# Optimization experiments

Hardware: AMD Instinct MI355X
Metric: run time of the kernel (lower is better)

Reference implementation:

```python
import jax, jax.numpy as jnp
import numpy as np

MAX_REL = 16  # max_relative_position (keys == values)


def _relative_positions(T, max_pos):
    r = jnp.arange(T)
    dist = r[None, :] - r[:, None]          # [T, T], k - q
    return jnp.clip(dist, -max_pos, max_pos) + max_pos


def setup_inputs() -> dict:
    key = jax.random.key(0)
    ks = jax.random.split(key, 5)
    B, H, T, D = 4, 16, 1024, 64
    V = 2 * MAX_REL + 1
    return {
        "q": jax.random.normal(ks[0], (B, H, T, D), jnp.float32),
        "k": jax.random.normal(ks[1], (B, H, T, D), jnp.float32),
        "v": jax.random.normal(ks[2], (B, H, T, D), jnp.float32),
        "emb_k": jax.random.normal(ks[3], (V, D), jnp.float32),
        "emb_v": jax.random.normal(ks[4], (V, D), jnp.float32),
    }


def reference(q, k, v, emb_k, emb_v):
    # q,k,v: [B,H,T,D]; emb_*: [2*MAX_REL+1, D]
    T = q.shape[2]
    D = k.shape[-1]
    rel_idx = _relative_positions(T, MAX_REL)          # [T,T]
    rel_k = emb_k[rel_idx]                             # [T,T,D]
    rel_v = emb_v[rel_idx]                             # [T,T,D]

    # content-content + content-position logits
    logits = jnp.einsum('bhtd,bhsd->bhts', q, k)
    logits = logits + jnp.einsum('bhtd,tsd->bhts', q, rel_k)
    logits = logits * (1.0 / jnp.sqrt(jnp.float32(D)))

    attn = jax.nn.softmax(logits, axis=-1)             # [B,H,T,T]
    out = jnp.einsum('bhts,bhsd->bhtd', attn, v)
    out = out + jnp.einsum('bhts,tsd->bhtd', attn, rel_v)
    return out, attn
```

## Files before the change

### kernel.cpp

```cpp
#include <hip/hip_runtime.h>
#include <hip/hip_bf16.h>

#define TT 1024
#define DD 64
#define MAXREL 16
#define NV 33
#define QBLK 16
#define SCALE 0.125f
#define BH 64

typedef short bf16x8 __attribute__((ext_vector_type(8)));
typedef short bf16x4 __attribute__((ext_vector_type(4)));
typedef float f32x4 __attribute__((ext_vector_type(4)));

#define SBAR() __builtin_amdgcn_sched_barrier(0)
#define WAITV(N)   __builtin_amdgcn_s_waitcnt(0x0F70 | (N))
#define WAITLGKM() __builtin_amdgcn_s_waitcnt(0xC07F)

static __device__ inline void gload16(const void* g, void* l) {
    __builtin_amdgcn_global_load_lds(
        (const __attribute__((address_space(1))) void*)g,
        (__attribute__((address_space(3))) void*)l, 16, 0, 0);
}

static __device__ inline short f2bf(float f) {
    __hip_bfloat16 h = __float2bfloat16(f);
    return *(short*)&h;
}
static __device__ inline float bf2f(short s) {
    union { unsigned u; float f; } x;
    x.u = ((unsigned)(unsigned short)s) << 16;
    return x.f;
}
static __device__ inline bf16x8 pack8(float4 a, float4 b) {
    bf16x8 r;
    r[0]=f2bf(a.x); r[1]=f2bf(a.y); r[2]=f2bf(a.z); r[3]=f2bf(a.w);
    r[4]=f2bf(b.x); r[5]=f2bf(b.y); r[6]=f2bf(b.z); r[7]=f2bf(b.w);
    return r;
}

__global__ __launch_bounds__(256)
void convk_kernel(const float* __restrict__ src, short* __restrict__ dst) {
    size_t i = (size_t)blockIdx.x * 256 + threadIdx.x;
    const float4* s = (const float4*)(src + i * 8);
    *(bf16x8*)(dst + i * 8) = pack8(s[0], s[1]);
}

__global__ __launch_bounds__(256)
void transv_kernel(const float* __restrict__ v, short* __restrict__ vt) {
    int bh = blockIdx.x >> 4;
    int st = blockIdx.x & 15;
    int wave = threadIdx.x >> 6, lane = threadIdx.x & 63;
    int s0 = st * 64 + wave * 16;
    const float* vp = v + ((size_t)bh * TT + s0) * DD + lane;
    bf16x8 lo, hi;
    #pragma unroll
    for (int e = 0; e < 8; ++e) lo[e] = f2bf(vp[(size_t)e * DD]);
    #pragma unroll
    for (int e = 0; e < 8; ++e) hi[e] = f2bf(vp[(size_t)(e + 8) * DD]);
    short* dp = vt + ((size_t)bh * DD + lane) * TT + s0;
    *(bf16x8*)dp = lo;
    *(bf16x8*)(dp + 8) = hi;
}

__global__ __launch_bounds__(512)
void relattn_kernel(const float* __restrict__ q_g,
                    const short* __restrict__ kb,
                    const short* __restrict__ vt,
                    const float* __restrict__ ek_g,
                    const float* __restrict__ ev_g,
                    float* __restrict__ out_g,
                    float* __restrict__ attn_g) {
    __shared__ __align__(16) char pbuf[QBLK * 2048];
    __shared__ __align__(16) char kstage[8 * 4096];
    __shared__ float pair_lds[4][16][16];
    __shared__ float qe_lds[QBLK * NV];
    __shared__ float w_lds[QBLK * NV];
    __shared__ float psum_lds[QBLK][8];
    __shared__ float psuf_lds[QBLK][8];
    __shared__ float pmid_lds[QBLK][8];
    __shared__ float inv_lds[QBLK];

    const int t    = threadIdx.x;
    const int bid  = blockIdx.x;
    const int wg   = ((bid & 7) << 9) | (bid >> 3);
    const int bh   = wg >> 6;
    const int q0   = (wg & 63) * QBLK;
    const int w    = t >> 6;
    const int lane = t & 63;
    const int lr   = lane & 15;
    const int akg  = lane >> 4;
    const int srl  = lane >> 3;
    const int sqg  = (lane & 7) ^ srl;

    const short* kgbase = kb + (size_t)bh * TT * DD;
    char* kst = kstage + w * 4096;

    auto KSTAGE = [&](int B, int NT) {
        const int s0 = w * 128 + NT * 16;
        gload16(kgbase + (size_t)(s0 + srl) * 64 + sqg * 8,     kst + B * 2048);
        gload16(kgbase + (size_t)(s0 + 8 + srl) * 64 + sqg * 8, kst + B * 2048 + 1024);
    };

    bf16x8 qF0, qF1;
    {
        const float* qp = q_g + ((size_t)bh * TT + q0 + lr) * DD + akg * 8;
        float4 a = *(const float4*)qp,        b = *(const float4*)(qp + 4);
        float4 c = *(const float4*)(qp + 32), d = *(const float4*)(qp + 36);
        qF0 = pack8(a, b); qF1 = pack8(c, d);
    }

    KSTAGE(0, 0); KSTAGE(1, 1);

    for (int i = t; i < QBLK * NV; i += 512) w_lds[i] = 0.f;
    if (w < 3) {
        int v = w * 16 + lr; if (v > 32) v = 32;
        const float* ep = ek_g + v * DD + akg * 8;
        float4 a = *(const float4*)ep,        b = *(const float4*)(ep + 4);
        float4 c = *(const float4*)(ep + 32), d = *(const float4*)(ep + 36);
        bf16x8 eF0 = pack8(a, b), eF1 = pack8(c, d);
        f32x4 qacc = {0.f, 0.f, 0.f, 0.f};
        qacc = __builtin_amdgcn_mfma_f32_16x16x32_bf16(eF0, qF0, qacc, 0, 0, 0);
        qacc = __builtin_amdgcn_mfma_f32_16x16x32_bf16(eF1, qF1, qacc, 0, 0, 0);
        #pragma unroll
        for (int j = 0; j < 4; ++j) {
            int vv = w * 16 + akg * 4 + j;
            if (vv < NV) qe_lds[lr * NV + vv] = __expf(qacc[j] * SCALE);
        }
    }
    __syncthreads();

    {
        const int tq = q0 + lr;
        const int X  = (lr & 7) << 4;
        const float eqe_lo = qe_lds[lr * NV];
        const float eqe_hi = qe_lds[lr * NV + 32];
        float sum = 0.f, suff = 0.f, msum = 0.f;

        auto CVALU = [&](f32x4 acc, int nt) {
            const int sb = w * 128 + nt * 16 + akg * 4;
            float ex0 = __expf(acc[0] * SCALE), ex1 = __expf(acc[1] * SCALE);
            float ex2 = __expf(acc[2] * SCALE), ex3 = __expf(acc[3] * SCALE);
            float e0, e1, e2, e3;
            if (sb >= tq + MAXREL) {
                e0 = ex0 * eqe_hi; e1 = ex1 * eqe_hi;
                e2 = ex2 * eqe_hi; e3 = ex3 * eqe_hi;
                float csum = (e0 + e1) + (e2 + e3);
                sum += csum; suff += csum;
            } else if (sb + 3 <= tq - MAXREL) {
                e0 = ex0 * eqe_lo; e1 = ex1 * eqe_lo;
                e2 = ex2 * eqe_lo; e3 = ex3 * eqe_lo;
                sum += (e0 + e1) + (e2 + e3);
            } else {
                float ee[4]; float exs[4] = {ex0, ex1, ex2, ex3};
                #pragma unroll
                for (int j = 0; j < 4; ++j) {
                    int dr = sb + j - tq;
                    int dc = dr < -MAXREL ? -MAXREL : (dr > MAXREL ? MAXREL : dr);
                    float v = exs[j] * qe_lds[lr * NV + dc + MAXREL];
                    ee[j] = v;
                    sum += v;
                    if (dr >= MAXREL) suff += v;
                    if (dr > -MAXREL && dr < MAXREL) {
                        w_lds[lr * NV + dr + MAXREL] = v;
                        msum += v;
                    }
                }
                e0 = ee[0]; e1 = ee[1]; e2 = ee[2]; e3 = ee[3];
            }
            bf16x4 p4;
            p4[0] = f2bf(e0); p4[1] = f2bf(e1);
            p4[2] = f2bf(e2); p4[3] = f2bf(e3);
            *(bf16x4*)(pbuf + lr * 2048 + ((2 * sb) ^ X)) = p4;
        };

        auto MFMA2 = [&](bf16x8 kf0, bf16x8 kf1) {
            f32x4 acc = {0.f, 0.f, 0.f, 0.f};
            acc = __builtin_amdgcn_mfma_f32_16x16x32_bf16(kf0, qF0, acc, 0, 0, 0);
            acc = __builtin_amdgcn_mfma_f32_16x16x32_bf16(kf1, qF1, acc, 0, 0, 0);
            return acc;
        };

        f32x4 aA, aB;
        #define CITER(B, NT, W, PF, AC, AP, NP) \
            WAITV(W); SBAR(); \
            { bf16x8 kf0 = *(const bf16x8*)(kst + (B)*2048 + lr*128 + ((((akg))  ^(lr&7)) << 4)); \
              bf16x8 kf1 = *(const bf16x8*)(kst + (B)*2048 + lr*128 + ((((akg)+4)^(lr&7)) << 4)); \
              if ((NP) >= 0) CVALU(AP, NP); \
              WAITLGKM(); SBAR(); \
              if (PF) KSTAGE((B), (NT) + 2); \
              AC = MFMA2(kf0, kf1); } \
            SBAR()
        CITER(0, 0, 2, 1, aA, aB, -1);
        CITER(1, 1, 2, 1, aB, aA,  0);
        CITER(0, 2, 2, 1, aA, aB,  1);
        CITER(1, 3, 2, 1, aB, aA,  2);
        CITER(0, 4, 2, 1, aA, aB,  3);
        CITER(1, 5, 2, 1, aB, aA,  4);
        CITER(0, 6, 2, 0, aA, aB,  5);
        CITER(1, 7, 0, 0, aB, aA,  6);
        CVALU(aB, 7);
        #undef CITER

        {
            WAITLGKM(); SBAR();
            const short* vgbase = vt + ((size_t)bh * DD + (w & 3) * 16) * TT;
            const int S0 = (w >> 2) * 8;
            gload16(vgbase + (size_t)srl * TT + S0 * 64 + sqg * 8,           kst);
            gload16(vgbase + (size_t)(8 + srl) * TT + S0 * 64 + sqg * 8,     kst + 1024);
            gload16(vgbase + (size_t)srl * TT + (S0 + 1) * 64 + sqg * 8,     kst + 2048);
            gload16(vgbase + (size_t)(8 + srl) * TT + (S0 + 1) * 64 + sqg * 8, kst + 3072);
        }

        sum  += __shfl_xor(sum, 16);  sum  += __shfl_xor(sum, 32);
        suff += __shfl_xor(suff, 16); suff += __shfl_xor(suff, 32);
        msum += __shfl_xor(msum, 16); msum += __shfl_xor(msum, 32);
        if (lane < 16) {
            psum_lds[lr][w] = sum;
            psuf_lds[lr][w] = suff;
            pmid_lds[lr][w] = msum;
        }
    }
    __syncthreads();

    if (t < QBLK) {
        float s = 0.f, sf = 0.f, sm = 0.f;
        #pragma unroll
        for (int i = 0; i < 8; ++i) {
            s  += psum_lds[t][i];
            sf += psuf_lds[t][i];
            sm += pmid_lds[t][i];
        }
        inv_lds[t] = 1.0f / s;
        w_lds[t * NV]      = s - sf - sm;
        w_lds[t * NV + 32] = sf;
    }
    __syncthreads();

    {
        const int dt = w & 3;
        const int sh = w >> 2;
        const int S0 = sh * 8;
        const int lc = lane & 15;
        const int dcol = dt * 16 + lc;
        const char* pb = pbuf + lc * 2048;
        const int X = (lc & 7) << 4;
        char* vst = kst;
        const short* vgbase = vt + ((size_t)bh * DD + dt * 16) * TT;
        f32x4 acc0 = {0.f, 0.f, 0.f, 0.f};
        f32x4 acc1 = {0.f, 0.f, 0.f, 0.f};

        auto VSTAGE = [&](int B, int S) {
            gload16(vgbase + (size_t)srl * TT + S * 64 + sqg * 8,       vst + B * 2048);
            gload16(vgbase + (size_t)(8 + srl) * TT + S * 64 + sqg * 8, vst + B * 2048 + 1024);
        };

        #define FITER(B, S, W, PF, AC) \
            WAITV(W); SBAR(); \
            { bf16x8 vf0 = *(const bf16x8*)(vst + (B)*2048 + lc*128 + ((((akg))  ^(lc&7)) << 4)); \
              bf16x8 vf1 = *(const bf16x8*)(vst + (B)*2048 + lc*128 + ((((akg)+4)^(lc&7)) << 4)); \
              bf16x8 a0 = *(const bf16x8*)(pb + (((2*(S))*64     + akg*16) ^ X)); \
              bf16x8 a1 = *(const bf16x8*)(pb + (((2*(S)+1)*64   + akg*16) ^ X)); \
              WAITLGKM(); SBAR(); \
              if (PF) VSTAGE((B), (S) + 2); \
              AC = __builtin_amdgcn_mfma_f32_16x16x32_bf16(a0, vf0, AC, 0, 0, 0); \
              AC = __builtin_amdgcn_mfma_f32_16x16x32_bf16(a1, vf1, AC, 0, 0, 0); } \
            SBAR()
        FITER(0, S0 + 0, 2, 1, acc0);  FITER(1, S0 + 1, 2, 1, acc1);
        FITER(0, S0 + 2, 2, 1, acc0);  FITER(1, S0 + 3, 2, 1, acc1);
        FITER(0, S0 + 4, 2, 1, acc0);  FITER(1, S0 + 5, 2, 1, acc1);
        FITER(0, S0 + 6, 2, 0, acc0);  FITER(1, S0 + 7, 0, 0, acc1);
        #undef FITER

        f32x4 acc;
        acc[0] = acc0[0] + acc1[0]; acc[1] = acc0[1] + acc1[1];
        acc[2] = acc0[2] + acc1[2]; acc[3] = acc0[3] + acc1[3];

        if (sh == 1) {
            #pragma unroll
            for (int j = 0; j < 4; ++j)
                pair_lds[dt][akg * 4 + j][lc] = acc[j];
        }
        __syncthreads();

        if (sh == 0) {
            const int rb = akg * 4;
            float o0 = acc[0] + pair_lds[dt][rb + 0][lc];
            float o1 = acc[1] + pair_lds[dt][rb + 1][lc];
            float o2 = acc[2] + pair_lds[dt][rb + 2][lc];
            float o3 = acc[3] + pair_lds[dt][rb + 3][lc];
            #pragma unroll 8
            for (int v = 0; v < NV; ++v) {
                float ev = ev_g[v * DD + dcol];
                o0 += w_lds[(rb + 0) * NV + v] * ev;
                o1 += w_lds[(rb + 1) * NV + v] * ev;
                o2 += w_lds[(rb + 2) * NV + v] * ev;
                o3 += w_lds[(rb + 3) * NV + v] * ev;
            }
            float* op = out_g + ((size_t)bh * TT + q0 + rb) * DD + dcol;
            op[0 * DD] = o0 * inv_lds[rb + 0];
            op[1 * DD] = o1 * inv_lds[rb + 1];
            op[2 * DD] = o2 * inv_lds[rb + 2];
            op[3 * DD] = o3 * inv_lds[rb + 3];
        }
    }

    {
        float* ab = attn_g + ((size_t)bh * TT + q0) * TT;
        #pragma unroll
        for (int j = 0; j < 2; ++j) {
            const int r = w * 2 + j;
            const float inv = inv_lds[r];
            const int X = (r & 7) << 4;
            #pragma unroll
            for (int i = 0; i < 4; ++i) {
                bf16x4 p4 = *(const bf16x4*)(pbuf + r * 2048 + ((8 * lane + 512 * i) ^ X));
                f32x4 o;
                o[0] = bf2f(p4[0]) * inv; o[1] = bf2f(p4[1]) * inv;
                o[2] = bf2f(p4[2]) * inv; o[3] = bf2f(p4[3]) * inv;
                __builtin_nontemporal_store(o, (f32x4*)(ab + (size_t)r * TT + lane * 4 + 256 * i));
            }
        }
    }
}

extern "C" void kernel_launch(void* const* d_in, const int* in_sizes, int n_in,
                              void* d_out, int out_size, void* d_ws, size_t ws_size,
                              hipStream_t stream) {
    const float* q  = (const float*)d_in[0];
    const float* k  = (const float*)d_in[1];
    const float* v  = (const float*)d_in[2];
    const float* ek = (const float*)d_in[3];
    const float* ev = (const float*)d_in[4];
    float* out  = (float*)d_out;
    float* attn = out + (size_t)BH * TT * DD;

    short* kbuf = (short*)d_ws;
    short* vtb  = kbuf + (size_t)BH * TT * DD;

    convk_kernel<<<dim3(2048), dim3(256), 0, stream>>>(k, kbuf);
    transv_kernel<<<dim3(1024), dim3(256), 0, stream>>>(v, vtb);
    relattn_kernel<<<dim3(4096), dim3(512), 0, stream>>>(q, kbuf, vtb, ek, ev, out, attn);
}
```

Before: 118.9 us.

## Replace LDS-staged K/V pipelines with direct global fragment loads for higher occupancy

```diff
diff --git a/kernel.cpp b/kernel.cpp
--- a/kernel.cpp
+++ b/kernel.cpp
@@ -12,16 +12,6 @@
 typedef short bf16x8 __attribute__((ext_vector_type(8)));
 typedef short bf16x4 __attribute__((ext_vector_type(4)));
 typedef float f32x4 __attribute__((ext_vector_type(4)));
-
-#define SBAR() __builtin_amdgcn_sched_barrier(0)
-#define WAITV(N)   __builtin_amdgcn_s_waitcnt(0x0F70 | (N))
-#define WAITLGKM() __builtin_amdgcn_s_waitcnt(0xC07F)
-
-static __device__ inline void gload16(const void* g, void* l) {
-    __builtin_amdgcn_global_load_lds(
-        (const __attribute__((address_space(1))) void*)g,
-        (__attribute__((address_space(3))) void*)l, 16, 0, 0);
-}
 
 static __device__ inline short f2bf(float f) {
     __hip_bfloat16 h = __float2bfloat16(f);
@@ -63,7 +53,7 @@
     *(bf16x8*)(dp + 8) = hi;
 }
 
-__global__ __launch_bounds__(512)
+__global__ __launch_bounds__(512, 8)
 void relattn_kernel(const float* __restrict__ q_g,
                     const short* __restrict__ kb,
                     const short* __restrict__ vt,
@@ -72,8 +62,7 @@
                     float* __restrict__ out_g,
                     float* __restrict__ attn_g) {
     __shared__ __align__(16) char pbuf[QBLK * 2048];
-    __shared__ __align__(16) char kstage[8 * 4096];
-    __shared__ float pair_lds[4][16][16];
+    __shared__ short pair_lds[4][16][16];
     __shared__ float qe_lds[QBLK * NV];
     __shared__ float w_lds[QBLK * NV];
     __shared__ float psum_lds[QBLK][8];
@@ -90,17 +79,6 @@
     const int lane = t & 63;
     const int lr   = lane & 15;
     const int akg  = lane >> 4;
-    const int srl  = lane >> 3;
-    const int sqg  = (lane & 7) ^ srl;
-
-    const short* kgbase = kb + (size_t)bh * TT * DD;
-    char* kst = kstage + w * 4096;
-
-    auto KSTAGE = [&](int B, int NT) {
-        const int s0 = w * 128 + NT * 16;
-        gload16(kgbase + (size_t)(s0 + srl) * 64 + sqg * 8,     kst + B * 2048);
-        gload16(kgbase + (size_t)(s0 + 8 + srl) * 64 + sqg * 8, kst + B * 2048 + 1024);
-    };
 
     bf16x8 qF0, qF1;
     {
@@ -109,8 +87,6 @@
         float4 c = *(const float4*)(qp + 32), d = *(const float4*)(qp + 36);
         qF0 = pack8(a, b); qF1 = pack8(c, d);
     }
-
-    KSTAGE(0, 0); KSTAGE(1, 1);
 
     for (int i = t; i < QBLK * NV; i += 512) w_lds[i] = 0.f;
     if (w < 3) {
@@ -131,13 +107,18 @@
     __syncthreads();
 
     {
+        const short* kp0 = kb + (size_t)bh * TT * DD
+                         + (size_t)(w * 128 + lr) * DD + akg * 8;
         const int tq = q0 + lr;
         const int X  = (lr & 7) << 4;
         const float eqe_lo = qe_lds[lr * NV];
         const float eqe_hi = qe_lds[lr * NV + 32];
         float sum = 0.f, suff = 0.f, msum = 0.f;
 
-        auto CVALU = [&](f32x4 acc, int nt) {
+        auto CCOMP = [&](bf16x8 kf0, bf16x8 kf1, int nt) {
+            f32x4 acc = {0.f, 0.f, 0.f, 0.f};
+            acc = __builtin_amdgcn_mfma_f32_16x16x32_bf16(kf0, qF0, acc, 0, 0, 0);
+            acc = __builtin_amdgcn_mfma_f32_16x16x32_bf16(kf1, qF1, acc, 0, 0, 0);
             const int sb = w * 128 + nt * 16 + akg * 4;
             float ex0 = __expf(acc[0] * SCALE), ex1 = __expf(acc[1] * SCALE);
             float ex2 = __expf(acc[2] * SCALE), ex3 = __expf(acc[3] * SCALE);
@@ -174,43 +155,20 @@
             *(bf16x4*)(pbuf + lr * 2048 + ((2 * sb) ^ X)) = p4;
         };
 
-        auto MFMA2 = [&](bf16x8 kf0, bf16x8 kf1) {
-            f32x4 acc = {0.f, 0.f, 0.f, 0.f};
-            acc = __builtin_amdgcn_mfma_f32_16x16x32_bf16(kf0, qF0, acc, 0, 0, 0);
-            acc = __builtin_amdgcn_mfma_f32_16x16x32_bf16(kf1, qF1, acc, 0, 0, 0);
-            return acc;
-        };
-
-        f32x4 aA, aB;
-        #define CITER(B, NT, W, PF, AC, AP, NP) \
-            WAITV(W); SBAR(); \
-            { bf16x8 kf0 = *(const bf16x8*)(kst + (B)*2048 + lr*128 + ((((akg))  ^(lr&7)) << 4)); \
-              bf16x8 kf1 = *(const bf16x8*)(kst + (B)*2048 + lr*128 + ((((akg)+4)^(lr&7)) << 4)); \
-              if ((NP) >= 0) CVALU(AP, NP); \
-              WAITLGKM(); SBAR(); \
-              if (PF) KSTAGE((B), (NT) + 2); \
-              AC = MFMA2(kf0, kf1); } \
-            SBAR()
-        CITER(0, 0, 2, 1, aA, aB, -1);
-        CITER(1, 1, 2, 1, aB, aA,  0);
-        CITER(0, 2, 2, 1, aA, aB,  1);
-        CITER(1, 3, 2, 1, aB, aA,  2);
-        CITER(0, 4, 2, 1, aA, aB,  3);
-        CITER(1, 5, 2, 1, aB, aA,  4);
-        CITER(0, 6, 2, 0, aA, aB,  5);
-        CITER(1, 7, 0, 0, aB, aA,  6);
-        CVALU(aB, 7);
-        #undef CITER
-
-        {
-            WAITLGKM(); SBAR();
-            const short* vgbase = vt + ((size_t)bh * DD + (w & 3) * 16) * TT;
-            const int S0 = (w >> 2) * 8;
-            gload16(vgbase + (size_t)srl * TT + S0 * 64 + sqg * 8,           kst);
-            gload16(vgbase + (size_t)(8 + srl) * TT + S0 * 64 + sqg * 8,     kst + 1024);
-            gload16(vgbase + (size_t)srl * TT + (S0 + 1) * 64 + sqg * 8,     kst + 2048);
-            gload16(vgbase + (size_t)(8 + srl) * TT + (S0 + 1) * 64 + sqg * 8, kst + 3072);
-        }
+        bf16x8 kA0, kA1, kB0, kB1;
+        #define KLD(R0, R1, NT) \
+            R0 = *(const bf16x8*)(kp0 + (NT) * 1024); \
+            R1 = *(const bf16x8*)(kp0 + (NT) * 1024 + 32)
+        KLD(kA0, kA1, 0); KLD(kB0, kB1, 1);
+        CCOMP(kA0, kA1, 0); KLD(kA0, kA1, 2);
+        CCOMP(kB0, kB1, 1); KLD(kB0, kB1, 3);
+        CCOMP(kA0, kA1, 2); KLD(kA0, kA1, 4);
+        CCOMP(kB0, kB1, 3); KLD(kB0, kB1, 5);
+        CCOMP(kA0, kA1, 4); KLD(kA0, kA1, 6);
+        CCOMP(kB0, kB1, 5); KLD(kB0, kB1, 7);
+        CCOMP(kA0, kA1, 6);
+        CCOMP(kB0, kB1, 7);
+        #undef KLD
 
         sum  += __shfl_xor(sum, 16);  sum  += __shfl_xor(sum, 32);
         suff += __shfl_xor(suff, 16); suff += __shfl_xor(suff, 32);
@@ -240,37 +198,29 @@
     {
         const int dt = w & 3;
         const int sh = w >> 2;
-        const int S0 = sh * 8;
         const int lc = lane & 15;
         const int dcol = dt * 16 + lc;
         const char* pb = pbuf + lc * 2048;
         const int X = (lc & 7) << 4;
-        char* vst = kst;
-        const short* vgbase = vt + ((size_t)bh * DD + dt * 16) * TT;
+        const short* vb = vt + ((size_t)bh * DD + dcol) * TT + sh * 512 + akg * 8;
         f32x4 acc0 = {0.f, 0.f, 0.f, 0.f};
         f32x4 acc1 = {0.f, 0.f, 0.f, 0.f};
 
-        auto VSTAGE = [&](int B, int S) {
-            gload16(vgbase + (size_t)srl * TT + S * 64 + sqg * 8,       vst + B * 2048);
-            gload16(vgbase + (size_t)(8 + srl) * TT + S * 64 + sqg * 8, vst + B * 2048 + 1024);
-        };
-
-        #define FITER(B, S, W, PF, AC) \
-            WAITV(W); SBAR(); \
-            { bf16x8 vf0 = *(const bf16x8*)(vst + (B)*2048 + lc*128 + ((((akg))  ^(lc&7)) << 4)); \
-              bf16x8 vf1 = *(const bf16x8*)(vst + (B)*2048 + lc*128 + ((((akg)+4)^(lc&7)) << 4)); \
-              bf16x8 a0 = *(const bf16x8*)(pb + (((2*(S))*64     + akg*16) ^ X)); \
-              bf16x8 a1 = *(const bf16x8*)(pb + (((2*(S)+1)*64   + akg*16) ^ X)); \
-              WAITLGKM(); SBAR(); \
-              if (PF) VSTAGE((B), (S) + 2); \
-              AC = __builtin_amdgcn_mfma_f32_16x16x32_bf16(a0, vf0, AC, 0, 0, 0); \
-              AC = __builtin_amdgcn_mfma_f32_16x16x32_bf16(a1, vf1, AC, 0, 0, 0); } \
-            SBAR()
-        FITER(0, S0 + 0, 2, 1, acc0);  FITER(1, S0 + 1, 2, 1, acc1);
-        FITER(0, S0 + 2, 2, 1, acc0);  FITER(1, S0 + 3, 2, 1, acc1);
-        FITER(0, S0 + 4, 2, 1, acc0);  FITER(1, S0 + 5, 2, 1, acc1);
-        FITER(0, S0 + 6, 2, 0, acc0);  FITER(1, S0 + 7, 0, 0, acc1);
-        #undef FITER
+        #pragma unroll
+        for (int g = 0; g < 4; ++g) {
+            bf16x8 v0 = *(const bf16x8*)(vb + (4*g+0) * 32);
+            bf16x8 v1 = *(const bf16x8*)(vb + (4*g+1) * 32);
+            bf16x8 v2 = *(const bf16x8*)(vb + (4*g+2) * 32);
+            bf16x8 v3 = *(const bf16x8*)(vb + (4*g+3) * 32);
+            bf16x8 a0 = *(const bf16x8*)(pb + ((sh*1024 + (4*g+0)*64 + akg*16) ^ X));
+            bf16x8 a1 = *(const bf16x8*)(pb + ((sh*1024 + (4*g+1)*64 + akg*16) ^ X));
+            bf16x8 a2 = *(const bf16x8*)(pb + ((sh*1024 + (4*g+2)*64 + akg*16) ^ X));
+            bf16x8 a3 = *(const bf16x8*)(pb + ((sh*1024 + (4*g+3)*64 + akg*16) ^ X));
+            acc0 = __builtin_amdgcn_mfma_f32_16x16x32_bf16(a0, v0, acc0, 0, 0, 0);
+            acc1 = __builtin_amdgcn_mfma_f32_16x16x32_bf16(a1, v1, acc1, 0, 0, 0);
+            acc0 = __builtin_amdgcn_mfma_f32_16x16x32_bf16(a2, v2, acc0, 0, 0, 0);
+            acc1 = __builtin_amdgcn_mfma_f32_16x16x32_bf16(a3, v3, acc1, 0, 0, 0);
+        }
 
         f32x4 acc;
         acc[0] = acc0[0] + acc1[0]; acc[1] = acc0[1] + acc1[1];
@@ -279,16 +229,16 @@
         if (sh == 1) {
             #pragma unroll
             for (int j = 0; j < 4; ++j)
-                pair_lds[dt][akg * 4 + j][lc] = acc[j];
+                pair_lds[dt][akg * 4 + j][lc] = f2bf(acc[j]);
         }
         __syncthreads();
 
         if (sh == 0) {
             const int rb = akg * 4;
-            float o0 = acc[0] + pair_lds[dt][rb + 0][lc];
-            float o1 = acc[1] + pair_lds[dt][rb + 1][lc];
-            float o2 = acc[2] + pair_lds[dt][rb + 2][lc];
-            float o3 = acc[3] + pair_lds[dt][rb + 3][lc];
+            float o0 = acc[0] + bf2f(pair_lds[dt][rb + 0][lc]);
+            float o1 = acc[1] + bf2f(pair_lds[dt][rb + 1][lc]);
+            float o2 = acc[2] + bf2f(pair_lds[dt][rb + 2][lc]);
+            float o3 = acc[3] + bf2f(pair_lds[dt][rb + 3][lc]);
             #pragma unroll 8
             for (int v = 0; v < NV; ++v) {
                 float ev = ev_g[v * DD + dcol];
```

Result: slower. 167.3 us (+40.7%).

## Shrink LDS footprint with single-buffered staging and bf16 scratch to raise occupancy

Applied to the files above, without the earlier changes.

```diff
diff --git a/kernel.cpp b/kernel.cpp
--- a/kernel.cpp
+++ b/kernel.cpp
@@ -14,7 +14,7 @@
 typedef float f32x4 __attribute__((ext_vector_type(4)));
 
 #define SBAR() __builtin_amdgcn_sched_barrier(0)
-#define WAITV(N)   __builtin_amdgcn_s_waitcnt(0x0F70 | (N))
+#define WAITV0()   __builtin_amdgcn_s_waitcnt(0x0F70)
 #define WAITLGKM() __builtin_amdgcn_s_waitcnt(0xC07F)
 
 static __device__ inline void gload16(const void* g, void* l) {
@@ -63,7 +63,7 @@
     *(bf16x8*)(dp + 8) = hi;
 }
 
-__global__ __launch_bounds__(512)
+__global__ __launch_bounds__(512, 6)
 void relattn_kernel(const float* __restrict__ q_g,
                     const short* __restrict__ kb,
                     const short* __restrict__ vt,
@@ -72,13 +72,13 @@
                     float* __restrict__ out_g,
                     float* __restrict__ attn_g) {
     __shared__ __align__(16) char pbuf[QBLK * 2048];
-    __shared__ __align__(16) char kstage[8 * 4096];
-    __shared__ float pair_lds[4][16][16];
-    __shared__ float qe_lds[QBLK * NV];
-    __shared__ float w_lds[QBLK * NV];
-    __shared__ float psum_lds[QBLK][8];
-    __shared__ float psuf_lds[QBLK][8];
-    __shared__ float pmid_lds[QBLK][8];
+    __shared__ __align__(16) char kstage[8 * 2048];
+    __shared__ short pair_lds[4][16][16];
+    __shared__ short qe_lds[QBLK * NV];
+    __shared__ short w_lds[QBLK * NV];
+    __shared__ short psum_lds[QBLK][8];
+    __shared__ short psuf_lds[QBLK][8];
+    __shared__ short pmid_lds[QBLK][8];
     __shared__ float inv_lds[QBLK];
 
     const int t    = threadIdx.x;
@@ -94,12 +94,12 @@
     const int sqg  = (lane & 7) ^ srl;
 
     const short* kgbase = kb + (size_t)bh * TT * DD;
-    char* kst = kstage + w * 4096;
-
-    auto KSTAGE = [&](int B, int NT) {
+    char* kst = kstage + w * 2048;
+
+    auto KSTAGE = [&](int NT) {
         const int s0 = w * 128 + NT * 16;
-        gload16(kgbase + (size_t)(s0 + srl) * 64 + sqg * 8,     kst + B * 2048);
-        gload16(kgbase + (size_t)(s0 + 8 + srl) * 64 + sqg * 8, kst + B * 2048 + 1024);
+        gload16(kgbase + (size_t)(s0 + srl) * 64 + sqg * 8,     kst);
+        gload16(kgbase + (size_t)(s0 + 8 + srl) * 64 + sqg * 8, kst + 1024);
     };
 
     bf16x8 qF0, qF1;
@@ -110,9 +110,9 @@
         qF0 = pack8(a, b); qF1 = pack8(c, d);
     }
 
-    KSTAGE(0, 0); KSTAGE(1, 1);
-
-    for (int i = t; i < QBLK * NV; i += 512) w_lds[i] = 0.f;
+    KSTAGE(0);
+
+    for (int i = t; i < QBLK * NV; i += 512) w_lds[i] = 0;
     if (w < 3) {
         int v = w * 16 + lr; if (v > 32) v = 32;
         const float* ep = ek_g + v * DD + akg * 8;
@@ -125,7 +125,7 @@
         #pragma unroll
         for (int j = 0; j < 4; ++j) {
             int vv = w * 16 + akg * 4 + j;
-            if (vv < NV) qe_lds[lr * NV + vv] = __expf(qacc[j] * SCALE);
+            if (vv < NV) qe_lds[lr * NV + vv] = f2bf(__expf(qacc[j] * SCALE));
         }
     }
     __syncthreads();
@@ -133,8 +133,8 @@
     {
         const int tq = q0 + lr;
         const int X  = (lr & 7) << 4;
-        const float eqe_lo = qe_lds[lr * NV];
-        const float eqe_hi = qe_lds[lr * NV + 32];
+        const float eqe_lo = bf2f(qe_lds[lr * NV]);
+        const float eqe_hi = bf2f(qe_lds[lr * NV + 32]);
         float sum = 0.f, suff = 0.f, msum = 0.f;
 
         auto CVALU = [&](f32x4 acc, int nt) {
@@ -157,12 +157,12 @@
                 for (int j = 0; j < 4; ++j) {
                     int dr = sb + j - tq;
                     int dc = dr < -MAXREL ? -MAXREL : (dr > MAXREL ? MAXREL : dr);
-                    float v = exs[j] * qe_lds[lr * NV + dc + MAXREL];
+                    float v = exs[j] * bf2f(qe_lds[lr * NV + dc + MAXREL]);
                     ee[j] = v;
                     sum += v;
                     if (dr >= MAXREL) suff += v;
                     if (dr > -MAXREL && dr < MAXREL) {
-                        w_lds[lr * NV + dr + MAXREL] = v;
+                        w_lds[lr * NV + dr + MAXREL] = f2bf(v);
                         msum += v;
                     }
                 }
@@ -182,43 +182,40 @@
         };
 
         f32x4 aA, aB;
-        #define CITER(B, NT, W, PF, AC, AP, NP) \
-            WAITV(W); SBAR(); \
-            { bf16x8 kf0 = *(const bf16x8*)(kst + (B)*2048 + lr*128 + ((((akg))  ^(lr&7)) << 4)); \
-              bf16x8 kf1 = *(const bf16x8*)(kst + (B)*2048 + lr*128 + ((((akg)+4)^(lr&7)) << 4)); \
+        #define CITER(NT, PF, AC, AP, NP) \
+            WAITV0(); SBAR(); \
+            { bf16x8 kf0 = *(const bf16x8*)(kst + lr*128 + ((((akg))  ^(lr&7)) << 4)); \
+              bf16x8 kf1 = *(const bf16x8*)(kst + lr*128 + ((((akg)+4)^(lr&7)) << 4)); \
               if ((NP) >= 0) CVALU(AP, NP); \
               WAITLGKM(); SBAR(); \
-              if (PF) KSTAGE((B), (NT) + 2); \
+              if (PF) KSTAGE((NT) + 1); \
               AC = MFMA2(kf0, kf1); } \
             SBAR()
-        CITER(0, 0, 2, 1, aA, aB, -1);
-        CITER(1, 1, 2, 1, aB, aA,  0);
-        CITER(0, 2, 2, 1, aA, aB,  1);
-        CITER(1, 3, 2, 1, aB, aA,  2);
-        CITER(0, 4, 2, 1, aA, aB,  3);
-        CITER(1, 5, 2, 1, aB, aA,  4);
-        CITER(0, 6, 2, 0, aA, aB,  5);
-        CITER(1, 7, 0, 0, aB, aA,  6);
+        CITER(0, 1, aA, aB, -1);
+        CITER(1, 1, aB, aA,  0);
+        CITER(2, 1, aA, aB,  1);
+        CITER(3, 1, aB, aA,  2);
+        CITER(4, 1, aA, aB,  3);
+        CITER(5, 1, aB, aA,  4);
+        CITER(6, 1, aA, aB,  5);
+        CITER(7, 0, aB, aA,  6);
         CVALU(aB, 7);
         #undef CITER
 
         {
-            WAITLGKM(); SBAR();
             const short* vgbase = vt + ((size_t)bh * DD + (w & 3) * 16) * TT;
             const int S0 = (w >> 2) * 8;
-            gload16(vgbase + (size_t)srl * TT + S0 * 64 + sqg * 8,           kst);
-            gload16(vgbase + (size_t)(8 + srl) * TT + S0 * 64 + sqg * 8,     kst + 1024);
-            gload16(vgbase + (size_t)srl * TT + (S0 + 1) * 64 + sqg * 8,     kst + 2048);
-            gload16(vgbase + (size_t)(8 + srl) * TT + (S0 + 1) * 64 + sqg * 8, kst + 3072);
+            gload16(vgbase + (size_t)srl * TT + S0 * 64 + sqg * 8,       kst);
+            gload16(vgbase + (size_t)(8 + srl) * TT + S0 * 64 + sqg * 8, kst + 1024);
         }
 
         sum  += __shfl_xor(sum, 16);  sum  += __shfl_xor(sum, 32);
         suff += __shfl_xor(suff, 16); suff += __shfl_xor(suff, 32);
         msum += __shfl_xor(msum, 16); msum += __shfl_xor(msum, 32);
         if (lane < 16) {
-            psum_lds[lr][w] = sum;
-            psuf_lds[lr][w] = suff;
-            pmid_lds[lr][w] = msum;
+            psum_lds[lr][w] = f2bf(sum);
+            psuf_lds[lr][w] = f2bf(suff);
+            pmid_lds[lr][w] = f2bf(msum);
         }
     }
     __syncthreads();
@@ -227,13 +224,13 @@
         float s = 0.f, sf = 0.f, sm = 0.f;
         #pragma unroll
         for (int i = 0; i < 8; ++i) {
-            s  += psum_lds[t][i];
-            sf += psuf_lds[t][i];
-            sm += pmid_lds[t][i];
+            s  += bf2f(psum_lds[t][i]);
+            sf += bf2f(psuf_lds[t][i]);
+            sm += bf2f(pmid_lds[t][i]);
         }
         inv_lds[t] = 1.0f / s;
-        w_lds[t * NV]      = s - sf - sm;
-        w_lds[t * NV + 32] = sf;
+        w_lds[t * NV]      = f2bf(s - sf - sm);
+        w_lds[t * NV + 32] = f2bf(sf);
     }
     __syncthreads();
 
@@ -250,26 +247,26 @@
         f32x4 acc0 = {0.f, 0.f, 0.f, 0.f};
         f32x4 acc1 = {0.f, 0.f, 0.f, 0.f};
 
-        auto VSTAGE = [&](int B, int S) {
-            gload16(vgbase + (size_t)srl * TT + S * 64 + sqg * 8,       vst + B * 2048);
-            gload16(vgbase + (size_t)(8 + srl) * TT + S * 64 + sqg * 8, vst + B * 2048 + 1024);
+        auto VSTAGE = [&](int S) {
+            gload16(vgbase + (size_t)srl * TT + S * 64 + sqg * 8,       vst);
+            gload16(vgbase + (size_t)(8 + srl) * TT + S * 64 + sqg * 8, vst + 1024);
         };
 
-        #define FITER(B, S, W, PF, AC) \
-            WAITV(W); SBAR(); \
-            { bf16x8 vf0 = *(const bf16x8*)(vst + (B)*2048 + lc*128 + ((((akg))  ^(lc&7)) << 4)); \
-              bf16x8 vf1 = *(const bf16x8*)(vst + (B)*2048 + lc*128 + ((((akg)+4)^(lc&7)) << 4)); \
+        #define FITER(S, PF, AC) \
+            WAITV0(); SBAR(); \
+            { bf16x8 vf0 = *(const bf16x8*)(vst + lc*128 + ((((akg))  ^(lc&7)) << 4)); \
+              bf16x8 vf1 = *(const bf16x8*)(vst + lc*128 + ((((akg)+4)^(lc&7)) << 4)); \
               bf16x8 a0 = *(const bf16x8*)(pb + (((2*(S))*64     + akg*16) ^ X)); \
               bf16x8 a1 = *(const bf16x8*)(pb + (((2*(S)+1)*64   + akg*16) ^ X)); \
               WAITLGKM(); SBAR(); \
-              if (PF) VSTAGE((B), (S) + 2); \
+              if (PF) VSTAGE((S) + 1); \
               AC = __builtin_amdgcn_mfma_f32_16x16x32_bf16(a0, vf0, AC, 0, 0, 0); \
               AC = __builtin_amdgcn_mfma_f32_16x16x32_bf16(a1, vf1, AC, 0, 0, 0); } \
             SBAR()
-        FITER(0, S0 + 0, 2, 1, acc0);  FITER(1, S0 + 1, 2, 1, acc1);
-        FITER(0, S0 + 2, 2, 1, acc0);  FITER(1, S0 + 3, 2, 1, acc1);
-        FITER(0, S0 + 4, 2, 1, acc0);  FITER(1, S0 + 5, 2, 1, acc1);
-        FITER(0, S0 + 6, 2, 0, acc0);  FITER(1, S0 + 7, 0, 0, acc1);
+        FITER(S0 + 0, 1, acc0);  FITER(S0 + 1, 1, acc1);
+        FITER(S0 + 2, 1, acc0);  FITER(S0 + 3, 1, acc1);
+        FITER(S0 + 4, 1, acc0);  FITER(S0 + 5, 1, acc1);
+        FITER(S0 + 6, 1, acc0);  FITER(S0 + 7, 0, acc1);
         #undef FITER
 
         f32x4 acc;
@@ -279,23 +276,23 @@
         if (sh == 1) {
             #pragma unroll
             for (int j = 0; j < 4; ++j)
-                pair_lds[dt][akg * 4 + j][lc] = acc[j];
+                pair_lds[dt][akg * 4 + j][lc] = f2bf(acc[j]);
         }
         __syncthreads();
 
         if (sh == 0) {
             const int rb = akg * 4;
-            float o0 = acc[0] + pair_lds[dt][rb + 0][lc];
-            float o1 = acc[1] + pair_lds[dt][rb + 1][lc];
-            float o2 = acc[2] + pair_lds[dt][rb + 2][lc];
-            float o3 = acc[3] + pair_lds[dt][rb + 3][lc];
+            float o0 = acc[0] + bf2f(pair_lds[dt][rb + 0][lc]);
+            float o1 = acc[1] + bf2f(pair_lds[dt][rb + 1][lc]);
+            float o2 = acc[2] + bf2f(pair_lds[dt][rb + 2][lc]);
+            float o3 = acc[3] + bf2f(pair_lds[dt][rb + 3][lc]);
             #pragma unroll 8
             for (int v = 0; v < NV; ++v) {
                 float ev = ev_g[v * DD + dcol];
-                o0 += w_lds[(rb + 0) * NV + v] * ev;
-                o1 += w_lds[(rb + 1) * NV + v] * ev;
-                o2 += w_lds[(rb + 2) * NV + v] * ev;
-                o3 += w_lds[(rb + 3) * NV + v] * ev;
+                o0 += bf2f(w_lds[(rb + 0) * NV + v]) * ev;
+                o1 += bf2f(w_lds[(rb + 1) * NV + v]) * ev;
+                o2 += bf2f(w_lds[(rb + 2) * NV + v]) * ev;
+                o3 += bf2f(w_lds[(rb + 3) * NV + v]) * ev;
             }
             float* op = out_g + ((size_t)bh * TT + q0 + rb) * DD + dcol;
             op[0 * DD] = o0 * inv_lds[rb + 0];
```

After: 132.1 us. +11.1%, slower.

## Keep softmax probabilities in registers and feed PV MFMA via lane shuffles

Applied to the files above, without the earlier changes.

```diff
diff --git a/kernel.cpp b/kernel.cpp
--- a/kernel.cpp
+++ b/kernel.cpp
@@ -31,6 +31,9 @@
     union { unsigned u; float f; } x;
     x.u = ((unsigned)(unsigned short)s) << 16;
     return x.f;
+}
+static __device__ inline unsigned pk2(float lo, float hi) {
+    return (unsigned)(unsigned short)f2bf(lo) | ((unsigned)(unsigned short)f2bf(hi) << 16);
 }
 static __device__ inline bf16x8 pack8(float4 a, float4 b) {
     bf16x8 r;
@@ -63,7 +66,7 @@
     *(bf16x8*)(dp + 8) = hi;
 }
 
-__global__ __launch_bounds__(512)
+__global__ __launch_bounds__(512, 6)
 void relattn_kernel(const float* __restrict__ q_g,
                     const short* __restrict__ kb,
                     const short* __restrict__ vt,
@@ -71,9 +74,7 @@
                     const float* __restrict__ ev_g,
                     float* __restrict__ out_g,
                     float* __restrict__ attn_g) {
-    __shared__ __align__(16) char pbuf[QBLK * 2048];
     __shared__ __align__(16) char kstage[8 * 4096];
-    __shared__ float pair_lds[4][16][16];
     __shared__ float qe_lds[QBLK * NV];
     __shared__ float w_lds[QBLK * NV];
     __shared__ float psum_lds[QBLK][8];
@@ -130,14 +131,15 @@
     }
     __syncthreads();
 
+    uint2 pP0, pP1, pP2, pP3, pP4, pP5, pP6, pP7;
+
     {
         const int tq = q0 + lr;
-        const int X  = (lr & 7) << 4;
         const float eqe_lo = qe_lds[lr * NV];
         const float eqe_hi = qe_lds[lr * NV + 32];
         float sum = 0.f, suff = 0.f, msum = 0.f;
 
-        auto CVALU = [&](f32x4 acc, int nt) {
+        auto CVALU = [&](f32x4 acc, int nt) -> uint2 {
             const int sb = w * 128 + nt * 16 + akg * 4;
             float ex0 = __expf(acc[0] * SCALE), ex1 = __expf(acc[1] * SCALE);
             float ex2 = __expf(acc[2] * SCALE), ex3 = __expf(acc[3] * SCALE);
@@ -168,10 +170,10 @@
                 }
                 e0 = ee[0]; e1 = ee[1]; e2 = ee[2]; e3 = ee[3];
             }
-            bf16x4 p4;
-            p4[0] = f2bf(e0); p4[1] = f2bf(e1);
-            p4[2] = f2bf(e2); p4[3] = f2bf(e3);
-            *(bf16x4*)(pbuf + lr * 2048 + ((2 * sb) ^ X)) = p4;
+            uint2 r;
+            r.x = pk2(e0, e1);
+            r.y = pk2(e2, e3);
+            return r;
         };
 
         auto MFMA2 = [&](bf16x8 kf0, bf16x8 kf1) {
@@ -182,35 +184,25 @@
         };
 
         f32x4 aA, aB;
-        #define CITER(B, NT, W, PF, AC, AP, NP) \
+        #define CITER(B, NT, W, PF, AC, AP, NP, PD) \
             WAITV(W); SBAR(); \
             { bf16x8 kf0 = *(const bf16x8*)(kst + (B)*2048 + lr*128 + ((((akg))  ^(lr&7)) << 4)); \
               bf16x8 kf1 = *(const bf16x8*)(kst + (B)*2048 + lr*128 + ((((akg)+4)^(lr&7)) << 4)); \
-              if ((NP) >= 0) CVALU(AP, NP); \
+              if ((NP) >= 0) PD = CVALU(AP, NP); \
               WAITLGKM(); SBAR(); \
               if (PF) KSTAGE((B), (NT) + 2); \
               AC = MFMA2(kf0, kf1); } \
             SBAR()
-        CITER(0, 0, 2, 1, aA, aB, -1);
-        CITER(1, 1, 2, 1, aB, aA,  0);
-        CITER(0, 2, 2, 1, aA, aB,  1);
-        CITER(1, 3, 2, 1, aB, aA,  2);
-        CITER(0, 4, 2, 1, aA, aB,  3);
-        CITER(1, 5, 2, 1, aB, aA,  4);
-        CITER(0, 6, 2, 0, aA, aB,  5);
-        CITER(1, 7, 0, 0, aB, aA,  6);
-        CVALU(aB, 7);
+        CITER(0, 0, 2, 1, aA, aB, -1, pP0);
+        CITER(1, 1, 2, 1, aB, aA,  0, pP0);
+        CITER(0, 2, 2, 1, aA, aB,  1, pP1);
+        CITER(1, 3, 2, 1, aB, aA,  2, pP2);
+        CITER(0, 4, 2, 1, aA, aB,  3, pP3);
+        CITER(1, 5, 2, 1, aB, aA,  4, pP4);
+        CITER(0, 6, 2, 0, aA, aB,  5, pP5);
+        CITER(1, 7, 0, 0, aB, aA,  6, pP6);
+        pP7 = CVALU(aB, 7);
         #undef CITER
-
-        {
-            WAITLGKM(); SBAR();
-            const short* vgbase = vt + ((size_t)bh * DD + (w & 3) * 16) * TT;
-            const int S0 = (w >> 2) * 8;
-            gload16(vgbase + (size_t)srl * TT + S0 * 64 + sqg * 8,           kst);
-            gload16(vgbase + (size_t)(8 + srl) * TT + S0 * 64 + sqg * 8,     kst + 1024);
-            gload16(vgbase + (size_t)srl * TT + (S0 + 1) * 64 + sqg * 8,     kst + 2048);
-            gload16(vgbase + (size_t)(8 + srl) * TT + (S0 + 1) * 64 + sqg * 8, kst + 3072);
-        }
 
         sum  += __shfl_xor(sum, 16);  sum  += __shfl_xor(sum, 32);
         suff += __shfl_xor(suff, 16); suff += __shfl_xor(suff, 32);
@@ -238,88 +230,76 @@
     __syncthreads();
 
     {
-        const int dt = w & 3;
-        const int sh = w >> 2;
-        const int S0 = sh * 8;
-        const int lc = lane & 15;
-        const int dcol = dt * 16 + lc;
-        const char* pb = pbuf + lc * 2048;
-        const int X = (lc & 7) << 4;
-        char* vst = kst;
-        const short* vgbase = vt + ((size_t)bh * DD + dt * 16) * TT;
-        f32x4 acc0 = {0.f, 0.f, 0.f, 0.f};
-        f32x4 acc1 = {0.f, 0.f, 0.f, 0.f};
-
-        auto VSTAGE = [&](int B, int S) {
-            gload16(vgbase + (size_t)srl * TT + S * 64 + sqg * 8,       vst + B * 2048);
-            gload16(vgbase + (size_t)(8 + srl) * TT + S * 64 + sqg * 8, vst + B * 2048 + 1024);
+        const float invr = inv_lds[lr];
+        float* ab = attn_g + ((size_t)(bh * TT + q0 + lr)) * TT + w * 128;
+        f32x4 acc0 = {0.f,0.f,0.f,0.f}, acc1 = {0.f,0.f,0.f,0.f};
+        f32x4 acc2 = {0.f,0.f,0.f,0.f}, acc3 = {0.f,0.f,0.f,0.f};
+        const int srcA = lr + ((akg & 1) << 5);
+        const int srcB = srcA + 16;
+        const bool useO = akg >= 2;
+        const short* vbase = vt + ((size_t)bh * DD + lr) * TT + w * 128 + akg * 8;
+
+        auto PVCHUNK = [&](uint2 E, uint2 O, int S) {
+            unsigned ex0 = (unsigned)__shfl((int)E.x, srcA), ey0 = (unsigned)__shfl((int)E.y, srcA);
+            unsigned ex1 = (unsigned)__shfl((int)E.x, srcB), ey1 = (unsigned)__shfl((int)E.y, srcB);
+            unsigned ox0 = (unsigned)__shfl((int)O.x, srcA), oy0 = (unsigned)__shfl((int)O.y, srcA);
+            unsigned ox1 = (unsigned)__shfl((int)O.x, srcB), oy1 = (unsigned)__shfl((int)O.y, srcB);
+            union { unsigned u[4]; bf16x8 v; } af;
+            af.u[0] = useO ? ox0 : ex0;
+            af.u[1] = useO ? oy0 : ey0;
+            af.u[2] = useO ? ox1 : ex1;
+            af.u[3] = useO ? oy1 : ey1;
+            const short* vb = vbase + S * 32;
+            bf16x8 v0 = *(const bf16x8*)(vb);
+            bf16x8 v1 = *(const bf16x8*)(vb + 16 * TT);
+            bf16x8 v2 = *(const bf16x8*)(vb + 32 * TT);
+            bf16x8 v3 = *(const bf16x8*)(vb + 48 * TT);
+            acc0 = __builtin_amdgcn_mfma_f32_16x16x32_bf16(af.v, v0, acc0, 0, 0, 0);
+            acc1 = __builtin_amdgcn_mfma_f32_16x16x32_bf16(af.v, v1, acc1, 0, 0, 0);
+            acc2 = __builtin_amdgcn_mfma_f32_16x16x32_bf16(af.v, v2, acc2, 0, 0, 0);
+            acc3 = __builtin_amdgcn_mfma_f32_16x16x32_bf16(af.v, v3, acc3, 0, 0, 0);
+            f32x4 o;
+            o[0] = bf2f((short)(E.x & 0xffff)) * invr;
+            o[1] = bf2f((short)(E.x >> 16))    * invr;
+            o[2] = bf2f((short)(E.y & 0xffff)) * invr;
+            o[3] = bf2f((short)(E.y >> 16))    * invr;
+            __builtin_nontemporal_store(o, (f32x4*)(ab + (2*S)*16 + akg*4));
+            o[0] = bf2f((short)(O.x & 0xffff)) * invr;
+            o[1] = bf2f((short)(O.x >> 16))    * invr;
+            o[2] = bf2f((short)(O.y & 0xffff)) * invr;
+            o[3] = bf2f((short)(O.y >> 16))    * invr;
+            __builtin_nontemporal_store(o, (f32x4*)(ab + (2*S+1)*16 + akg*4));
         };
 
-        #define FITER(B, S, W, PF, AC) \
-            WAITV(W); SBAR(); \
-            { bf16x8 vf0 = *(const bf16x8*)(vst + (B)*2048 + lc*128 + ((((akg))  ^(lc&7)) << 4)); \
-              bf16x8 vf1 = *(const bf16x8*)(vst + (B)*2048 + lc*128 + ((((akg)+4)^(lc&7)) << 4)); \
-              bf16x8 a0 = *(const bf16x8*)(pb + (((2*(S))*64     + akg*16) ^ X)); \
-              bf16x8 a1 = *(const bf16x8*)(pb + (((2*(S)+1)*64   + akg*16) ^ X)); \
-              WAITLGKM(); SBAR(); \
-              if (PF) VSTAGE((B), (S) + 2); \
-              AC = __builtin_amdgcn_mfma_f32_16x16x32_bf16(a0, vf0, AC, 0, 0, 0); \
-              AC = __builtin_amdgcn_mfma_f32_16x16x32_bf16(a1, vf1, AC, 0, 0, 0); } \
-            SBAR()
-        FITER(0, S0 + 0, 2, 1, acc0);  FITER(1, S0 + 1, 2, 1, acc1);
-        FITER(0, S0 + 2, 2, 1, acc0);  FITER(1, S0 + 3, 2, 1, acc1);
-        FITER(0, S0 + 4, 2, 1, acc0);  FITER(1, S0 + 5, 2, 1, acc1);
-        FITER(0, S0 + 6, 2, 0, acc0);  FITER(1, S0 + 7, 0, 0, acc1);
-        #undef FITER
-
-        f32x4 acc;
-        acc[0] = acc0[0] + acc1[0]; acc[1] = acc0[1] + acc1[1];
-        acc[2] = acc0[2] + acc1[2]; acc[3] = acc0[3] + acc1[3];
-
-        if (sh == 1) {
+        PVCHUNK(pP0, pP1, 0);
+        PVCHUNK(pP2, pP3, 1);
+        PVCHUNK(pP4, pP5, 2);
+        PVCHUNK(pP6, pP7, 3);
+
+        float* pw = (float*)kstage + w * 1024;
+        #pragma unroll
+        for (int j = 0; j < 4; ++j) {
+            pw[(akg*4 + j) * 64 +  0 + lr] = acc0[j];
+            pw[(akg*4 + j) * 64 + 16 + lr] = acc1[j];
+            pw[(akg*4 + j) * 64 + 32 + lr] = acc2[j];
+            pw[(akg*4 + j) * 64 + 48 + lr] = acc3[j];
+        }
+    }
+    __syncthreads();
+
+    {
+        const int d = t & 63;
+        const float* pr = (const float*)kstage;
+        #pragma unroll
+        for (int h = 0; h < 2; ++h) {
+            const int r = (t >> 6) + h * 8;
+            float o = 0.f;
             #pragma unroll
-            for (int j = 0; j < 4; ++j)
-                pair_lds[dt][akg * 4 + j][lc] = acc[j];
-        }
-        __syncthreads();
-
-        if (sh == 0) {
-            const int rb = akg * 4;
-            float o0 = acc[0] + pair_lds[dt][rb + 0][lc];
-            float o1 = acc[1] + pair_lds[dt][rb + 1][lc];
-            float o2 = acc[2] + pair_lds[dt][rb + 2][lc];
-            float o3 = acc[3] + pair_lds[dt][rb + 3][lc];
+            for (int ww = 0; ww < 8; ++ww) o += pr[ww * 1024 + r * 64 + d];
             #pragma unroll 8
-            for (int v = 0; v < NV; ++v) {
-                float ev = ev_g[v * DD + dcol];
-                o0 += w_lds[(rb + 0) * NV + v] * ev;
-                o1 += w_lds[(rb + 1) * NV + v] * ev;
-                o2 += w_lds[(rb + 2) * NV + v] * ev;
-                o3 += w_lds[(rb + 3) * NV + v] * ev;
-            }
-            float* op = out_g + ((size_t)bh * TT + q0 + rb) * DD + dcol;
-            op[0 * DD] = o0 * inv_lds[rb + 0];
-            op[1 * DD] = o1 * inv_lds[rb + 1];
-            op[2 * DD] = o2 * inv_lds[rb + 2];
-            op[3 * DD] = o3 * inv_lds[rb + 3];
-        }
-    }
-
-    {
-        float* ab = attn_g + ((size_t)bh * TT + q0) * TT;
-        #pragma unroll
-        for (int j = 0; j < 2; ++j) {
-            const int r = w * 2 + j;
-            const float inv = inv_lds[r];
-            const int X = (r & 7) << 4;
-            #pragma unroll
-            for (int i = 0; i < 4; ++i) {
-                bf16x4 p4 = *(const bf16x4*)(pbuf + r * 2048 + ((8 * lane + 512 * i) ^ X));
-                f32x4 o;
-                o[0] = bf2f(p4[0]) * inv; o[1] = bf2f(p4[1]) * inv;
-                o[2] = bf2f(p4[2]) * inv; o[3] = bf2f(p4[3]) * inv;
-                __builtin_nontemporal_store(o, (f32x4*)(ab + (size_t)r * TT + lane * 4 + 256 * i));
-            }
+            for (int v = 0; v < NV; ++v)
+                o += w_lds[r * NV + v] * ev_g[v * DD + d];
+            out_g[((size_t)bh * TT + q0 + r) * DD + d] = o * inv_lds[r];
         }
     }
 }
```

After: 155.7 us. +30.9%, slower.
